# Kernel optimization log

Measured on AMD Instinct MI355X. Metric: run time of the kernel, lower is better.

Reference implementation:

```python
import jax, jax.numpy as jnp
import numpy as np

N, E, DIM, H = 100000, 1600000, 128, 8
HD = DIM // H  # head_dim


def setup_inputs() -> dict:
    key = jax.random.key(0)
    ks = jax.random.split(key, 12)
    s = lambda k, sh, fan: jax.random.normal(k, sh, jnp.float32) * (1.0 / np.sqrt(fan))
    return {
        "x": jax.random.normal(ks[0], (N, DIM), jnp.float32),
        "src": jax.random.randint(ks[1], (E,), 0, N, jnp.int32),
        "dst": jax.random.randint(ks[2], (E,), 0, N, jnp.int32),
        # input_linear: dim -> dim
        "w_in": s(ks[3], (DIM, DIM), DIM), "b_in": jnp.zeros((DIM,), jnp.float32),
        # attn_linear_u: dim -> H (with bias); attn_linear_v: dim -> H (no bias)
        "w_au": s(ks[4], (DIM, H), DIM), "b_au": jnp.zeros((H,), jnp.float32),
        "w_av": s(ks[5], (DIM, H), DIM),
        # feed-forward: dim -> dim (hidden_dim_multiplier=1) -> dim
        "w1": s(ks[6], (DIM, DIM), DIM), "b1": jnp.zeros((DIM,), jnp.float32),
        "w2": s(ks[7], (DIM, DIM), DIM), "b2": jnpp if False else jnp.zeros((DIM,), jnp.float32),
    }


def reference(x, src, dst, w_in, b_in, w_au, b_au, w_av, w1, b1, w2, b2):
    n = x.shape[0]
    h = x @ w_in + b_in                      # [N, dim]
    a_u = h @ w_au + b_au                    # [N, H]
    a_v = h @ w_av                           # [N, H]
    # u_add_v: per-edge scores, then LeakyReLU(0.2)
    scores = jax.nn.leaky_relu(a_u[src] + a_v[dst], negative_slope=0.2)  # [E, H]
    # edge_softmax: normalize over incoming edges of each dst node
    smax = jax.ops.segment_max(scores, dst, num_segments=n)              # [N, H]
    ex = jnp.exp(scores - smax[dst])                                     # [E, H]
    denom = jax.ops.segment_sum(ex, dst, num_segments=n)                 # [N, H]
    probs = ex / denom[dst]                                              # [E, H]
    # u_mul_e_sum with x reshaped to [N, head_dim, H]
    hv = h.reshape(n, HD, H)
    msg = hv[src] * probs[:, None, :]                                    # [E, HD, H]
    agg = jax.ops.segment_sum(msg, dst, num_segments=n)                  # [N, HD, H]
    out = agg.reshape(n, DIM)
    # feed-forward (dropout=0, eval)
    out = jax.nn.gelu(out @ w1 + b1) @ w2 + b2
    return out
```

## Files before the change

### kernel.cpp

```cpp
#include <hip/hip_runtime.h>
#include <hip/hip_bf16.h>
#include <stdint.h>

#define DIM 128
#define NH 8
#define CH 4096
#define BK 128
#define LS 136

using bf16 = __hip_bfloat16;
typedef __attribute__((ext_vector_type(8))) short short8;
typedef __attribute__((ext_vector_type(4))) float floatx4;


__device__ inline float bf2f(unsigned short b) {
    return __uint_as_float(((unsigned)b) << 16);
}
__device__ inline unsigned short f2bf(float f) {
    unsigned u = __float_as_uint(f);
    u += 0x7FFFu + ((u >> 16) & 1u);
    return (unsigned short)(u >> 16);
}

__device__ inline float gelu_tanh(float x) {
    float x3 = x * x * x;
    float u = 0.7978845608028654f * (x + 0.044715f * x3);
    float e = __expf(2.f * u);
    float t = 1.f - 2.f / (e + 1.f);
    return 0.5f * x * (1.f + t);
}

__launch_bounds__(256)
__global__ void preconv_kernel(const float* __restrict__ w_in, const float* __restrict__ w1,
                               const float* __restrict__ w2, const float* __restrict__ w_au,
                               const float* __restrict__ w_av,
                               unsigned short* __restrict__ w_in_b, unsigned short* __restrict__ w1_b,
                               unsigned short* __restrict__ w2_b, unsigned short* __restrict__ wc_b) {
    const int b = blockIdx.x, tid = threadIdx.x;
    if (b < 12) {
        const int m = b >> 2, qtr = b & 3;
        const float* W = m == 0 ? w_in : (m == 1 ? w1 : w2);
        unsigned short* O = m == 0 ? w_in_b : (m == 1 ? w1_b : w2_b);
        const bool perm = (m == 1);
        #pragma unroll
        for (int i = 0; i < 16; ++i) {
            int o = qtr * 4096 + tid + i * 256;
            int k = o & 127, n = o >> 7;
            int krow = perm ? ((k & 15) * 8 + (k >> 4)) : k;
            O[o] = f2bf(W[krow * 128 + n]);
        }
    } else {
        #pragma unroll
        for (int i = 0; i < 8; ++i) {
            int o = tid + i * 256;
            int j = o >> 7, kt = o & 127;
            int ko = (kt & 15) * 8 + (kt >> 4);
            float v = (j < 8) ? w_au[ko * 8 + j] : w_av[ko * 8 + (j - 8)];
            wc_b[o] = f2bf(v);
        }
    }
}

__device__ __forceinline__ void stage_pre(unsigned short* wt, const unsigned short* __restrict__ pre,
                                          int tid) {
    #pragma unroll
    for (int i = 0; i < 4; ++i) {
        int g = tid + i * 512;
        short8 v = *(const short8*)(pre + g * 8);
        *(short8*)(wt + (g >> 4) * LS + (g & 15) * 8) = v;
    }
}

__launch_bounds__(512)
__global__ void gemm_in_attn_kernel(const float* __restrict__ x, const unsigned short* __restrict__ w_in_b,
                                    const float* __restrict__ b_in,
                                    const unsigned short* __restrict__ wc_b, const float* __restrict__ b_au,
                                    bf16* __restrict__ h, float* __restrict__ au,
                                    float* __restrict__ av, int M) {
    __shared__ __align__(16) unsigned short wt[128 * LS];
    __shared__ __align__(16) unsigned short wc[16 * LS];
    const int tid = threadIdx.x;

    stage_pre(wt, w_in_b, tid);
    {
        int j = tid >> 5, kt4 = (tid & 31) * 4;
        const unsigned* s = (const unsigned*)(wc_b + j * 128 + kt4);
        unsigned* d = (unsigned*)(wc + j * LS + kt4);
        d[0] = s[0]; d[1] = s[1];
    }
    __syncthreads();

    const int wave = tid >> 6;
    const int lane = tid & 63;
    const int l15 = lane & 15;
    const int q = lane >> 4;
    const int rowbase = blockIdx.x * 128 + wave * 16;
    const int rowA = min(rowbase + l15, M - 1);

    floatx4 acc[8];
    #pragma unroll
    for (int c = 0; c < 8; ++c) acc[c] = (floatx4){0.f, 0.f, 0.f, 0.f};

    #pragma unroll
    for (int kk = 0; kk < 4; ++kk) {
        const float* ap = x + (size_t)rowA * 128 + kk * 32 + q * 8;
        floatx4 a0 = *(const floatx4*)ap;
        floatx4 a1 = *(const floatx4*)(ap + 4);
        union { short8 s; unsigned short u[8]; } cv;
        #pragma unroll
        for (int j = 0; j < 4; ++j) { cv.u[j] = f2bf(a0[j]); cv.u[4 + j] = f2bf(a1[j]); }
        short8 afrag = cv.s;
        #pragma unroll
        for (int c = 0; c < 8; ++c) {
            short8 bfrag = *(const short8*)(wt + (c * 16 + l15) * LS + kk * 32 + q * 8);
            acc[c] = __builtin_amdgcn_mfma_f32_16x16x32_bf16(afrag, bfrag, acc[c], 0, 0, 0);
        }
    }
    __syncthreads();

    const int rl0 = wave * 16 + q * 4;
    #pragma unroll
    for (int c = 0; c < 8; ++c) {
        int col = c * 16 + l15;
        int colw = (col & 7) * 16 + (col >> 3);
        float b = b_in[col];
        #pragma unroll
        for (int r = 0; r < 4; ++r)
            wt[(rl0 + r) * LS + colw] = f2bf(acc[c][r] + b);
    }
    __syncthreads();

    const int blk0 = blockIdx.x * 128;
    #pragma unroll
    for (int i = 0; i < 4; ++i) {
        int g = tid + i * 512;
        int row = g >> 4;
        if (blk0 + row < M) {
            short8 v = *(const short8*)(wt + row * LS + (g & 15) * 8);
            *(short8*)((unsigned short*)h + (size_t)(blk0 + row) * 128 + (g & 15) * 8) = v;
        }
    }

    floatx4 acc2 = (floatx4){0.f, 0.f, 0.f, 0.f};
    #pragma unroll
    for (int kk = 0; kk < 4; ++kk) {
        short8 af = *(const short8*)(wt + (wave * 16 + l15) * LS + kk * 32 + q * 8);
        short8 bf = *(const short8*)(wc + l15 * LS + kk * 32 + q * 8);
        acc2 = __builtin_amdgcn_mfma_f32_16x16x32_bf16(af, bf, acc2, 0, 0, 0);
    }
    {
        const int row0 = rowbase + q * 4;
        int col = l15;
        #pragma unroll
        for (int r = 0; r < 4; ++r) {
            int rr = row0 + r;
            if (rr < M) {
                if (col < 8) au[(size_t)rr * 8 + col] = acc2[r] + b_au[col];
                else         av[(size_t)rr * 8 + (col - 8)] = acc2[r];
            }
        }
    }
}

__launch_bounds__(512)
__global__ void ff_kernel(const bf16* __restrict__ A, const unsigned short* __restrict__ w1_b,
                          const float* __restrict__ b1, const unsigned short* __restrict__ w2_b,
                          const float* __restrict__ b2, float* __restrict__ out, int M) {
    __shared__ __align__(16) unsigned short wt[128 * LS];
    __shared__ __align__(16) unsigned short ht[128 * LS];
    const int tid = threadIdx.x;

    stage_pre(wt, w1_b, tid);
    __syncthreads();

    const int wave = tid >> 6;
    const int lane = tid & 63;
    const int l15 = lane & 15;
    const int q = lane >> 4;
    const int rowbase = blockIdx.x * 128 + wave * 16;
    const int rowA = min(rowbase + l15, M - 1);

    floatx4 acc[8];
    #pragma unroll
    for (int c = 0; c < 8; ++c) acc[c] = (floatx4){0.f, 0.f, 0.f, 0.f};

    #pragma unroll
    for (int kk = 0; kk < 4; ++kk) {
        short8 afrag = *(const short8*)((const unsigned short*)A + (size_t)rowA * 128 + kk * 32 + q * 8);
        #pragma unroll
        for (int c = 0; c < 8; ++c) {
            short8 bfrag = *(const short8*)(wt + (c * 16 + l15) * LS + kk * 32 + q * 8);
            acc[c] = __builtin_amdgcn_mfma_f32_16x16x32_bf16(afrag, bfrag, acc[c], 0, 0, 0);
        }
    }
    __syncthreads();

    stage_pre(wt, w2_b, tid);
    const int rl0 = wave * 16 + q * 4;
    #pragma unroll
    for (int c = 0; c < 8; ++c) {
        int col = c * 16 + l15;
        float b = b1[col];
        #pragma unroll
        for (int r = 0; r < 4; ++r)
            ht[(rl0 + r) * LS + col] = f2bf(gelu_tanh(acc[c][r] + b));
    }
    __syncthreads();

    floatx4 acc2[8];
    #pragma unroll
    for (int c = 0; c < 8; ++c) acc2[c] = (floatx4){0.f, 0.f, 0.f, 0.f};
    #pragma unroll
    for (int kk = 0; kk < 4; ++kk) {
        short8 af = *(const short8*)(ht + (wave * 16 + l15) * LS + kk * 32 + q * 8);
        #pragma unroll
        for (int c = 0; c < 8; ++c) {
            short8 bfrag = *(const short8*)(wt + (c * 16 + l15) * LS + kk * 32 + q * 8);
            acc2[c] = __builtin_amdgcn_mfma_f32_16x16x32_bf16(af, bfrag, acc2[c], 0, 0, 0);
        }
    }

    const int row0 = rowbase + q * 4;
    #pragma unroll
    for (int c = 0; c < 8; ++c) {
        int col = c * 16 + l15;
        float b = b2[col];
        #pragma unroll
        for (int r = 0; r < 4; ++r) {
            int rr = row0 + r;
            if (rr < M) out[(size_t)rr * 128 + col] = acc2[c][r] + b;
        }
    }
}


__launch_bounds__(256)
__global__ void bucket_count_kernel(const int* __restrict__ dst, int* __restrict__ mat,
                                    int E, int K, int B) {
    __shared__ int cnt[1024];
    const int b = blockIdx.x;
    for (int k = threadIdx.x; k < K; k += 256) cnt[k] = 0;
    __syncthreads();
    const int base = b * CH, end = min(base + CH, E);
    for (int i = base + threadIdx.x; i < end; i += 256)
        atomicAdd(&cnt[dst[i] >> 7], 1);
    __syncthreads();
    for (int k = threadIdx.x; k < K; k += 256) mat[(size_t)k * B + b] = cnt[k];
}

__launch_bounds__(64)
__global__ void scan_bucket_kernel(int* __restrict__ mat, int* __restrict__ btot, int B) {
    const int k = blockIdx.x;
    const int lane = threadIdx.x;
    const size_t base = (size_t)k * B;
    int carry = 0;
    for (int i0 = 0; i0 < B; i0 += 64) {
        int idx = i0 + lane;
        int v = (idx < B) ? mat[base + idx] : 0;
        int incl = v;
        #pragma unroll
        for (int off = 1; off < 64; off <<= 1) {
            int y = __shfl_up(incl, off);
            if (lane >= off) incl += y;
        }
        int tot = __shfl(incl, 63);
        if (idx < B) mat[base + idx] = carry + incl - v;
        carry += tot;
    }
    if (lane == 0) btot[k] = carry;
}

__launch_bounds__(64)
__global__ void scan_total_kernel(const int* __restrict__ btot, int* __restrict__ bbase, int K) {
    const int lane = threadIdx.x;
    int carry = 0;
    for (int i0 = 0; i0 < K; i0 += 64) {
        int idx = i0 + lane;
        int v = (idx < K) ? btot[idx] : 0;
        int incl = v;
        #pragma unroll
        for (int off = 1; off < 64; off <<= 1) {
            int y = __shfl_up(incl, off);
            if (lane >= off) incl += y;
        }
        int tot = __shfl(incl, 63);
        if (idx < K) bbase[idx] = carry + incl - v;
        carry += tot;
    }
}

__launch_bounds__(256)
__global__ void bucket_scatter_kernel(const int* __restrict__ src, const int* __restrict__ dst,
                                      const int* __restrict__ mat, const int* __restrict__ bbase,
                                      unsigned* __restrict__ packed, int E, int K, int B) {
    __shared__ int cur[1024];
    const int b = blockIdx.x;
    for (int k = threadIdx.x; k < K; k += 256)
        cur[k] = bbase[k] + mat[(size_t)k * B + b];
    __syncthreads();
    const int base = b * CH, end = min(base + CH, E);
    for (int i = base + threadIdx.x; i < end; i += 256) {
        int d = dst[i], s = src[i];
        int pos = atomicAdd(&cur[d >> 7], 1);
        packed[pos] = (unsigned)s | ((unsigned)(d & 127) << 20);
    }
}

__launch_bounds__(256)
__global__ void bucket_csr_kernel(const unsigned* __restrict__ packed,
                                  const int* __restrict__ bbase, const int* __restrict__ btot,
                                  int* __restrict__ rowptr, int* __restrict__ deg,
                                  int* __restrict__ esrc, int N) {
    __shared__ int hist[128], cur[128];
    __shared__ int wtot;
    const int k = blockIdx.x;
    const int tid = threadIdx.x;
    const int lane = tid & 63;
    const int start = bbase[k];
    const int cnt = btot[k];

    if (tid < 128) hist[tid] = 0;
    __syncthreads();
    for (int i = tid; i < cnt; i += 256)
        atomicAdd(&hist[packed[start + i] >> 20], 1);
    __syncthreads();

    int v = (tid < 128) ? hist[tid] : 0;
    int incl = v;
    #pragma unroll
    for (int off = 1; off < 64; off <<= 1) {
        int y = __shfl_up(incl, off);
        if (lane >= off) incl += y;
    }
    if (tid == 63) wtot = incl;
    __syncthreads();
    int excl = incl - v + ((tid >= 64 && tid < 128) ? wtot : 0);
    if (tid < 128) {
        int n = k * BK + tid;
        if (n < N) { rowptr[n] = start + excl; deg[n] = v; }
        cur[tid] = excl;
    }
    __syncthreads();

    for (int i = tid; i < cnt; i += 256) {
        unsigned p = packed[start + i];
        int pos = atomicAdd(&cur[p >> 20], 1);
        esrc[start + pos] = (int)(p & 0xFFFFFu);
    }
}


__device__ __forceinline__ void unpack8fma(uint4 w, float p, float* o) {
    o[0] = fmaf(p, __uint_as_float(w.x << 16), o[0]);
    o[1] = fmaf(p, __uint_as_float(w.x & 0xFFFF0000u), o[1]);
    o[2] = fmaf(p, __uint_as_float(w.y << 16), o[2]);
    o[3] = fmaf(p, __uint_as_float(w.y & 0xFFFF0000u), o[3]);
    o[4] = fmaf(p, __uint_as_float(w.z << 16), o[4]);
    o[5] = fmaf(p, __uint_as_float(w.z & 0xFFFF0000u), o[5]);
    o[6] = fmaf(p, __uint_as_float(w.w << 16), o[6]);
    o[7] = fmaf(p, __uint_as_float(w.w & 0xFFFF0000u), o[7]);
}

template <bool MASKED>
__device__ __forceinline__ void do8e(const int* __restrict__ ep, int i, int nd,
                                     int e, int head, int d0b,
                                     const float* __restrict__ au,
                                     const char* __restrict__ hpb,
                                     float avh, float& l, float* o) {
    int idx = i + e;
    int s;
    float m = 1.f;
    if constexpr (MASKED) {
        s = ep[min(idx, nd - 1)];
        m = idx < nd ? 1.f : 0.f;
    } else {
        s = ep[idx];
    }
    float a = au[(s << 3) + head];
    size_t off = ((size_t)(unsigned)s) << 8;
    uint4 w0 = *(const uint4*)(hpb + off + d0b);
    uint4 w1 = *(const uint4*)(hpb + off + d0b + 16);
    float x = a + avh;
    x = fmaxf(x, 0.2f * x);
    float p = __expf(x);
    if constexpr (MASKED) p *= m;
    l += p;
    unpack8fma(w0, p, o);
    unpack8fma(w1, p, o + 8);
}

__launch_bounds__(256)
__global__ void agg_csr_kernel(const int* __restrict__ rowptr, const int* __restrict__ deg,
                               const int* __restrict__ esrc,
                               const float* __restrict__ au, const float* __restrict__ av,
                               const bf16* __restrict__ h, bf16* __restrict__ agg, int N) {
    const int node = (blockIdx.x * 256 + threadIdx.x) >> 6;
    if (node >= N) return;
    const int lane = threadIdx.x & 63;
    const int e = lane >> 3;
    const int head = lane & 7;
    const int d0b = head * 32;
    const char* hpb = (const char*)h;
    const int nd = deg[node];
    const int start = rowptr[node];
    const float avh = av[((size_t)node << 3) + head];
    const int* ep = esrc + start;

    float l0 = 0.f;
    float o[16];
    #pragma unroll
    for (int j = 0; j < 16; ++j) o[j] = 0.f;

    int i = 0;
    for (; i + 16 <= nd; i += 16) {
        do8e<false>(ep, i, nd, e, head, d0b, au, hpb, avh, l0, o);
        do8e<false>(ep, i + 8, nd, e, head, d0b, au, hpb, avh, l0, o);
    }
    if (i + 8 <= nd) { do8e<false>(ep, i, nd, e, head, d0b, au, hpb, avh, l0, o); i += 8; }
    if (i < nd) do8e<true>(ep, i, nd, e, head, d0b, au, hpb, avh, l0, o);

    #pragma unroll
    for (int j = 0; j < 16; ++j) {
        o[j] += __shfl_xor(o[j], 8);
        o[j] += __shfl_xor(o[j], 16);
        o[j] += __shfl_xor(o[j], 32);
    }
    l0 += __shfl_xor(l0, 8);
    l0 += __shfl_xor(l0, 16);
    l0 += __shfl_xor(l0, 32);

    if (lane < 8) {
        float inv = l0 > 0.f ? 1.f / l0 : 0.f;
        unsigned r[8];
        #pragma unroll
        for (int j = 0; j < 8; ++j)
            r[j] = ((unsigned)f2bf(o[2 * j + 1] * inv) << 16) | (unsigned)f2bf(o[2 * j] * inv);
        char* outp = (char*)agg + ((size_t)node << 8) + lane * 32;
        *(uint4*)outp = (uint4){r[0], r[1], r[2], r[3]};
        *(uint4*)(outp + 16) = (uint4){r[4], r[5], r[6], r[7]};
    }
}

extern "C" void kernel_launch(void* const* d_in, const int* in_sizes, int n_in,
                              void* d_out, int out_size, void* d_ws, size_t ws_size,
                              hipStream_t stream) {
    const float* x    = (const float*)d_in[0];
    const int*   src  = (const int*)d_in[1];
    const int*   dst  = (const int*)d_in[2];
    const float* w_in = (const float*)d_in[3];
    const float* b_in = (const float*)d_in[4];
    const float* w_au = (const float*)d_in[5];
    const float* b_au = (const float*)d_in[6];
    const float* w_av = (const float*)d_in[7];
    const float* w1   = (const float*)d_in[8];
    const float* b1   = (const float*)d_in[9];
    const float* w2   = (const float*)d_in[10];
    const float* b2   = (const float*)d_in[11];
    const int N = in_sizes[0] / DIM;
    const int E = in_sizes[1];
    const int K = (N + BK - 1) / BK;
    const int B = (E + CH - 1) / CH;

    char* p = (char*)d_ws;
    int*  deg    = (int*)p;  p += (size_t)N * 4;
    int*  rowptr = (int*)p;  p += (size_t)N * 4;
    int*  esrc   = (int*)p;  p += (size_t)E * 4;
    bf16* h      = (bf16*)p; p += (size_t)N * DIM * 2;
    float* au    = (float*)p; p += (size_t)N * NH * 4;
    float* av    = (float*)p; p += (size_t)N * NH * 4;
    unsigned short* w_in_b = (unsigned short*)p; p += 128 * 128 * 2;
    unsigned short* w1_b   = (unsigned short*)p; p += 128 * 128 * 2;
    unsigned short* w2_b   = (unsigned short*)p; p += 128 * 128 * 2;
    unsigned short* wc_b   = (unsigned short*)p; p += 16 * 128 * 2;
    bf16* agg    = (bf16*)p;  p += (size_t)N * DIM * 2;
    unsigned* packed = (unsigned*)agg;
    int* mat   = (int*)((char*)agg + (size_t)E * 4);
    int* btot  = mat + (size_t)K * B;
    int* bbase = btot + K;

    const int row_blocks = (N + 127) / 128;

    preconv_kernel<<<13, 256, 0, stream>>>(w_in, w1, w2, w_au, w_av, w_in_b, w1_b, w2_b, wc_b);

    gemm_in_attn_kernel<<<row_blocks, 512, 0, stream>>>(x, w_in_b, b_in, wc_b, b_au, h, au, av, N);

    bucket_count_kernel<<<B, 256, 0, stream>>>(dst, mat, E, K, B);
    scan_bucket_kernel<<<K, 64, 0, stream>>>(mat, btot, B);
    scan_total_kernel<<<1, 64, 0, stream>>>(btot, bbase, K);
    bucket_scatter_kernel<<<B, 256, 0, stream>>>(src, dst, mat, bbase, packed, E, K, B);
    bucket_csr_kernel<<<K, 256, 0, stream>>>(packed, bbase, btot, rowptr, deg, esrc, N);

    agg_csr_kernel<<<(N + 3) / 4, 256, 0, stream>>>(rowptr, deg, esrc, au, av, h, agg, N);

    ff_kernel<<<row_blocks, 512, 0, stream>>>(agg, w1_b, b1, w2_b, b2, (float*)d_out, N);
}
```

Baseline: 306.8 us.

## Scatter edges chunk-locally and gather buckets into LDS for CSR build

The bucket scatter now writes each edge chunk's packed entries in bucket-sorted order inside the chunk's own region, recording per-chunk bucket offsets, instead of scattering them to global bucket positions. The CSR kernel then gathers its bucket's segments from every chunk into a shared-memory buffer and does the histogram and placement from LDS. This aims to make the scatter writes more local and to avoid re-reading packed data from global memory twice. The bucket-count pass is also merged into the weight-conversion launch to drop one kernel. The trade-off is a serial per-thread gather loop over all chunks in the CSR kernel, and an LDS buffer that assumes no bucket exceeds 4096 edges.

```diff
diff --git a/kernel.cpp b/kernel.cpp
--- a/kernel.cpp
+++ b/kernel.cpp
@@ -7,6 +7,7 @@
 #define CH 4096
 #define BK 128
 #define LS 136
+#define EBUF 4096
 
 using bf16 = __hip_bfloat16;
 typedef __attribute__((ext_vector_type(8))) short short8;
@@ -31,32 +32,46 @@
 }
 
 __launch_bounds__(256)
-__global__ void preconv_kernel(const float* __restrict__ w_in, const float* __restrict__ w1,
-                               const float* __restrict__ w2, const float* __restrict__ w_au,
-                               const float* __restrict__ w_av,
-                               unsigned short* __restrict__ w_in_b, unsigned short* __restrict__ w1_b,
-                               unsigned short* __restrict__ w2_b, unsigned short* __restrict__ wc_b) {
+__global__ void count_pre_kernel(const int* __restrict__ dst, int* __restrict__ mat,
+                                 int E, int K, int B,
+                                 const float* __restrict__ w_in, const float* __restrict__ w1,
+                                 const float* __restrict__ w2, const float* __restrict__ w_au,
+                                 const float* __restrict__ w_av,
+                                 unsigned short* __restrict__ w_in_b, unsigned short* __restrict__ w1_b,
+                                 unsigned short* __restrict__ w2_b, unsigned short* __restrict__ wc_b) {
+    __shared__ int cnt[1024];
     const int b = blockIdx.x, tid = threadIdx.x;
-    if (b < 12) {
-        const int m = b >> 2, qtr = b & 3;
-        const float* W = m == 0 ? w_in : (m == 1 ? w1 : w2);
-        unsigned short* O = m == 0 ? w_in_b : (m == 1 ? w1_b : w2_b);
-        const bool perm = (m == 1);
-        #pragma unroll
-        for (int i = 0; i < 16; ++i) {
-            int o = qtr * 4096 + tid + i * 256;
-            int k = o & 127, n = o >> 7;
-            int krow = perm ? ((k & 15) * 8 + (k >> 4)) : k;
-            O[o] = f2bf(W[krow * 128 + n]);
-        }
+    if (b < B) {
+        for (int k = tid; k < K; k += 256) cnt[k] = 0;
+        __syncthreads();
+        const int base = b * CH, end = min(base + CH, E);
+        for (int i = base + tid; i < end; i += 256)
+            atomicAdd(&cnt[dst[i] >> 7], 1);
+        __syncthreads();
+        for (int k = tid; k < K; k += 256) mat[(size_t)k * B + b] = cnt[k];
     } else {
-        #pragma unroll
-        for (int i = 0; i < 8; ++i) {
-            int o = tid + i * 256;
-            int j = o >> 7, kt = o & 127;
-            int ko = (kt & 15) * 8 + (kt >> 4);
-            float v = (j < 8) ? w_au[ko * 8 + j] : w_av[ko * 8 + (j - 8)];
-            wc_b[o] = f2bf(v);
+        int pb = b - B;
+        if (pb < 12) {
+            const int m = pb >> 2, qtr = pb & 3;
+            const float* W = m == 0 ? w_in : (m == 1 ? w1 : w2);
+            unsigned short* O = m == 0 ? w_in_b : (m == 1 ? w1_b : w2_b);
+            const bool perm = (m == 1);
+            #pragma unroll
+            for (int i = 0; i < 16; ++i) {
+                int o = qtr * 4096 + tid + i * 256;
+                int k = o & 127, n = o >> 7;
+                int krow = perm ? ((k & 15) * 8 + (k >> 4)) : k;
+                O[o] = f2bf(W[krow * 128 + n]);
+            }
+        } else {
+            #pragma unroll
+            for (int i = 0; i < 8; ++i) {
+                int o = tid + i * 256;
+                int j = o >> 7, kt = o & 127;
+                int ko = (kt & 15) * 8 + (kt >> 4);
+                float v = (j < 8) ? w_au[ko * 8 + j] : w_av[ko * 8 + (j - 8)];
+                wc_b[o] = f2bf(v);
+            }
         }
     }
 }
@@ -233,20 +248,6 @@
     }
 }
 
-
-__launch_bounds__(256)
-__global__ void bucket_count_kernel(const int* __restrict__ dst, int* __restrict__ mat,
-                                    int E, int K, int B) {
-    __shared__ int cnt[1024];
-    const int b = blockIdx.x;
-    for (int k = threadIdx.x; k < K; k += 256) cnt[k] = 0;
-    __syncthreads();
-    const int base = b * CH, end = min(base + CH, E);
-    for (int i = base + threadIdx.x; i < end; i += 256)
-        atomicAdd(&cnt[dst[i] >> 7], 1);
-    __syncthreads();
-    for (int k = threadIdx.x; k < K; k += 256) mat[(size_t)k * B + b] = cnt[k];
-}
 
 __launch_bounds__(64)
 __global__ void scan_bucket_kernel(int* __restrict__ mat, int* __restrict__ btot, int B) {
@@ -291,40 +292,78 @@
 
 __launch_bounds__(256)
 __global__ void bucket_scatter_kernel(const int* __restrict__ src, const int* __restrict__ dst,
-                                      const int* __restrict__ mat, const int* __restrict__ bbase,
-                                      unsigned* __restrict__ packed, int E, int K, int B) {
+                                      int* __restrict__ lofs, unsigned* __restrict__ packed,
+                                      int E, int K, int B) {
+    __shared__ int hist[1024];
     __shared__ int cur[1024];
-    const int b = blockIdx.x;
-    for (int k = threadIdx.x; k < K; k += 256)
-        cur[k] = bbase[k] + mat[(size_t)k * B + b];
+    __shared__ int wsum[4];
+    const int b = blockIdx.x, tid = threadIdx.x;
+    for (int k = tid; k < 1024; k += 256) hist[k] = 0;
     __syncthreads();
     const int base = b * CH, end = min(base + CH, E);
-    for (int i = base + threadIdx.x; i < end; i += 256) {
+    for (int i = base + tid; i < end; i += 256)
+        atomicAdd(&hist[dst[i] >> 7], 1);
+    __syncthreads();
+    int v[4]; int t = 0;
+    #pragma unroll
+    for (int j = 0; j < 4; ++j) { int x = hist[tid * 4 + j]; v[j] = t; t += x; }
+    const int lane = tid & 63, wv = tid >> 6;
+    int incl = t;
+    #pragma unroll
+    for (int off = 1; off < 64; off <<= 1) {
+        int y = __shfl_up(incl, off);
+        if (lane >= off) incl += y;
+    }
+    if (lane == 63) wsum[wv] = incl;
+    __syncthreads();
+    int woff = 0;
+    #pragma unroll
+    for (int w = 0; w < 4; ++w) if (w < wv) woff += wsum[w];
+    int texcl = woff + incl - t;
+    #pragma unroll
+    for (int j = 0; j < 4; ++j) {
+        int k = tid * 4 + j;
+        int e = texcl + v[j];
+        cur[k] = e;
+        if (k < K) lofs[(size_t)b * K + k] = e;
+    }
+    __syncthreads();
+    for (int i = base + tid; i < end; i += 256) {
         int d = dst[i], s = src[i];
         int pos = atomicAdd(&cur[d >> 7], 1);
-        packed[pos] = (unsigned)s | ((unsigned)(d & 127) << 20);
+        packed[(size_t)b * CH + pos] = (unsigned)s | ((unsigned)(d & 127) << 20);
     }
 }
 
 __launch_bounds__(256)
-__global__ void bucket_csr_kernel(const unsigned* __restrict__ packed,
+__global__ void bucket_csr_kernel(const unsigned* __restrict__ packed, const int* __restrict__ lofs,
+                                  const int* __restrict__ mat,
                                   const int* __restrict__ bbase, const int* __restrict__ btot,
                                   int* __restrict__ rowptr, int* __restrict__ deg,
-                                  int* __restrict__ esrc, int N) {
+                                  int* __restrict__ esrc, int N, int E, int K, int B) {
+    __shared__ unsigned ebuf[EBUF];
     __shared__ int hist[128], cur[128];
     __shared__ int wtot;
-    const int k = blockIdx.x;
-    const int tid = threadIdx.x;
-    const int lane = tid & 63;
+    const int k = blockIdx.x, tid = threadIdx.x;
     const int start = bbase[k];
     const int cnt = btot[k];
 
+    for (int b = tid; b < B; b += 256) {
+        int lo = lofs[(size_t)b * K + k];
+        int chunk_len = min(CH, E - b * CH);
+        int hi = (k + 1 < K) ? lofs[(size_t)b * K + k + 1] : chunk_len;
+        int dbase = mat[(size_t)k * B + b];
+        const unsigned* sp = packed + (size_t)b * CH;
+        for (int j = lo; j < hi; ++j) ebuf[dbase + (j - lo)] = sp[j];
+    }
     if (tid < 128) hist[tid] = 0;
     __syncthreads();
+
     for (int i = tid; i < cnt; i += 256)
-        atomicAdd(&hist[packed[start + i] >> 20], 1);
-    __syncthreads();
-
+        atomicAdd(&hist[ebuf[i] >> 20], 1);
+    __syncthreads();
+
+    const int lane = tid & 63;
     int v = (tid < 128) ? hist[tid] : 0;
     int incl = v;
     #pragma unroll
@@ -343,7 +382,7 @@
     __syncthreads();
 
     for (int i = tid; i < cnt; i += 256) {
-        unsigned p = packed[start + i];
+        unsigned p = ebuf[i];
         int pos = atomicAdd(&cur[p >> 20], 1);
         esrc[start + pos] = (int)(p & 0xFFFFFu);
     }
@@ -474,21 +513,24 @@
     unsigned short* wc_b   = (unsigned short*)p; p += 16 * 128 * 2;
     bf16* agg    = (bf16*)p;  p += (size_t)N * DIM * 2;
     unsigned* packed = (unsigned*)agg;
-    int* mat   = (int*)((char*)agg + (size_t)E * 4);
+    int* mat   = (int*)((char*)agg + (size_t)B * CH * 4);
     int* btot  = mat + (size_t)K * B;
     int* bbase = btot + K;
+    int* lofs  = bbase + K;
 
     const int row_blocks = (N + 127) / 128;
 
-    preconv_kernel<<<13, 256, 0, stream>>>(w_in, w1, w2, w_au, w_av, w_in_b, w1_b, w2_b, wc_b);
+    count_pre_kernel<<<B + 13, 256, 0, stream>>>(dst, mat, E, K, B,
+                                                 w_in, w1, w2, w_au, w_av,
+                                                 w_in_b, w1_b, w2_b, wc_b);
 
     gemm_in_attn_kernel<<<row_blocks, 512, 0, stream>>>(x, w_in_b, b_in, wc_b, b_au, h, au, av, N);
 
-    bucket_count_kernel<<<B, 256, 0, stream>>>(dst, mat, E, K, B);
     scan_bucket_kernel<<<K, 64, 0, stream>>>(mat, btot, B);
     scan_total_kernel<<<1, 64, 0, stream>>>(btot, bbase, K);
-    bucket_scatter_kernel<<<B, 256, 0, stream>>>(src, dst, mat, bbase, packed, E, K, B);
-    bucket_csr_kernel<<<K, 256, 0, stream>>>(packed, bbase, btot, rowptr, deg, esrc, N);
+    bucket_scatter_kernel<<<B, 256, 0, stream>>>(src, dst, lofs, packed, E, K, B);
+    bucket_csr_kernel<<<K, 256, 0, stream>>>(packed, lofs, mat, bbase, btot,
+                                             rowptr, deg, esrc, N, E, K, B);
 
     agg_csr_kernel<<<(N + 3) / 4, 256, 0, stream>>>(rowptr, deg, esrc, au, av, h, agg, N);
 
```

New measurement: 295.6 us. 3.6% less time.
